# Kernel optimization log

Hardware: AMD Instinct MI355X
Metric: run time of the kernel (lower is better)

Reference implementation:

```python
import jax, jax.numpy as jnp
import numpy as np
import math

SENTINEL = 1.0e6  # eta/phi value assigned to inactive (pt<=0) objects
BIG = 1.0e6       # dR placeholder for non-lower-triangular entries


def _remove_duplicates(objs, threshold):
    """objs: (B, n, 3) with columns (pt, eta, phi). Zeros out objects that
    are within dR < threshold of a later object in the group (faithful to
    the TF strictly-lower-triangular / reduce over rows logic)."""
    n = objs.shape[1]
    active = objs[..., 0] > 0.0                              # (B, n)
    eta = jnp.where(active, objs[..., 1], SENTINEL)
    phi = jnp.where(active, objs[..., 2], SENTINEL)
    deta = eta[:, :, None] - eta[:, None, :]                 # (B, n, n)
    dphi = jnp.mod(phi[:, :, None] - phi[:, None, :] + math.pi,
                   2.0 * math.pi) - math.pi
    dr2 = deta * deta + dphi * dphi
    # strictly lower triangular mask (row i > col j), same as
    # logical_not(band_part(ones, 0, -1)) in TF
    tri = jnp.tril(jnp.ones((n, n), dtype=bool), k=-1)       # (n, n)
    # safe sqrt: only evaluate where the mask keeps the value
    dr = jnp.sqrt(jnp.where(tri, dr2, 1.0))
    replaced = jnp.where(tri, dr, BIG)                       # (B, n, n)
    # TF reduce_any(..., axis=0) per event -> axis=1 of batched tensor
    duplicates = jnp.any(replaced < threshold, axis=1)       # (B, n)
    return jnp.where(duplicates[..., None], 0.0, objs)


def duplicate_removal(x, threshold):
    jets = _remove_duplicates(x[:, 0:6], threshold)
    electrons = _remove_duplicates(x[:, 6:9], threshold)
    muons = _remove_duplicates(x[:, 9:12], threshold)
    photons = _remove_duplicates(x[:, 12:15], threshold)
    met = x[:, 15:16]
    return jnp.concatenate([jets, electrons, muons, photons, met], axis=1)


def setup_inputs() -> dict:
    key = jax.random.key(0)
    x = jax.random.normal(key, (1000000, 16, 3), dtype=jnp.float32)
    return {"x": x}


def reference(x):
    return duplicate_removal(x, 0.05)
```

## Files before the change

kernel.cpp:

```cpp
#include <hip/hip_runtime.h>
#include <math.h>

#define PI_F        3.14159274101257324e0f
#define TWOPI_F     6.28318548202514648e0f
#define TWOPI_D     ((double)TWOPI_F)
#define INV_TWOPI_D (1.0 / (double)TWOPI_F)

#define ROWS_PER_BLOCK 128
#define ROW_STRIDE     49

__device__ __forceinline__ int pair_close(float ei, float ej, float pi_, float pj) {
    float deta = __fsub_rn(ei, ej);
    float dd   = __fadd_rn(__fsub_rn(pi_, pj), PI_F);
    double ddd = (double)dd;
    double q   = trunc(ddd * INV_TWOPI_D);
    float  m   = (float)fma(-q, TWOPI_D, ddd);
    if (m < 0.0f) m = __fadd_rn(m, TWOPI_F);
    float dphi = __fsub_rn(m, PI_F);
    float dr2  = __fadd_rn(__fmul_rn(deta, deta), __fmul_rn(dphi, dphi));
    return __fsqrt_rn(dr2) < 0.05f;
}

template <int OFF, int N>
__device__ __forceinline__ unsigned group_dup(const float* r) {
    float e[N], p[N];
    int   a[N];
#pragma unroll
    for (int k = 0; k < N; ++k) {
        float pt = r[3 * (OFF + k) + 0];
        a[k] = pt > 0.0f;
        e[k] = r[3 * (OFF + k) + 1];
        p[k] = r[3 * (OFF + k) + 2];
    }
    unsigned dup = 0;
#pragma unroll
    for (int j = 0; j < N - 1; ++j) {
        int d = 0;
#pragma unroll
        for (int i = j + 1; i < N; ++i) {
            int close = pair_close(e[i], e[j], p[i], p[j]);
            d |= (a[i] & a[j] & close) | ((a[i] | a[j]) ^ 1);
        }
        if (d) dup |= (1u << (OFF + j));
    }
    return dup;
}

__global__ __launch_bounds__(256, 6) void dup_removal_kernel(
    const float4* __restrict__ in, float4* __restrict__ out, int B) {
    __shared__ float rowbuf[ROWS_PER_BLOCK * ROW_STRIDE];
    __shared__ unsigned long long maskbuf[ROWS_PER_BLOCK];

    const int t = threadIdx.x;
    const long long base4  = (long long)blockIdx.x * (ROWS_PER_BLOCK * 12);
    const long long total4 = (long long)B * 12;

    float4 v[6];
#pragma unroll
    for (int i = 0; i < 6; ++i) {
        long long g = base4 + t + 256 * i;
        if (g < total4) {
            v[i] = in[g];
            int local = t + 256 * i;
            int rl = local / 12;
            int f  = local - rl * 12;
            float* dstp = &rowbuf[rl * ROW_STRIDE + 4 * f];
            dstp[0] = v[i].x; dstp[1] = v[i].y; dstp[2] = v[i].z; dstp[3] = v[i].w;
        }
    }
    __syncthreads();

    if (t < ROWS_PER_BLOCK) {
        int row = blockIdx.x * ROWS_PER_BLOCK + t;
        unsigned dup = 0;
        if (row < B) {
            const float* r = rowbuf + t * ROW_STRIDE;
            dup  = group_dup<0, 6>(r);
            dup |= group_dup<6, 3>(r);
            dup |= group_dup<9, 3>(r);
            dup |= group_dup<12, 3>(r);
        }
        unsigned long long fm = 0ull;
#pragma unroll
        for (int o = 0; o < 15; ++o)
            fm |= (unsigned long long)((dup >> o) & 1u) * (7ull << (3 * o));
        maskbuf[t] = fm;
    }
    __syncthreads();

#pragma unroll
    for (int i = 0; i < 6; ++i) {
        long long g = base4 + t + 256 * i;
        if (g < total4) {
            int local = t + 256 * i;
            int rl = local / 12;
            int f  = local - rl * 12;
            unsigned nib = (unsigned)(maskbuf[rl] >> (4 * f)) & 0xFu;
            float4 w = v[i];
            if (nib & 1u) w.x = 0.0f;
            if (nib & 2u) w.y = 0.0f;
            if (nib & 4u) w.z = 0.0f;
            if (nib & 8u) w.w = 0.0f;
            out[g] = w;
        }
    }
}

extern "C" void kernel_launch(void* const* d_in, const int* in_sizes, int n_in,
                              void* d_out, int out_size, void* d_ws, size_t ws_size,
                              hipStream_t stream) {
    const float4* x = (const float4*)d_in[0];
    float4* out = (float4*)d_out;
    int B = in_sizes[0] / 48;
    int grid = (B + ROWS_PER_BLOCK - 1) / ROWS_PER_BLOCK;
    dup_removal_kernel<<<grid, 256, 0, stream>>>(x, out, B);
}
```

Measured before the change: 320.9 us.

## Use fp32 phi wrap, squared-distance compare, transposed LDS layout, full-block fast path

Replaces the double-precision mod computation with single-precision truncf/fma and compares squared distance against 0.0025 rather than taking a sqrt. The shared-memory row layout becomes field-strided (stride 12) so the compute-phase reads and the float4 stores conflict less across banks. A templated FULL path drops bounds checks for interior blocks, and launch bounds occupancy drops from 6 to 4. The fp32 mod and the squared compare can differ from the reference near boundaries.

```diff
diff --git a/kernel.cpp b/kernel.cpp
--- a/kernel.cpp
+++ b/kernel.cpp
@@ -3,8 +3,9 @@
 
 #define PI_F        3.14159274101257324e0f
 #define TWOPI_F     6.28318548202514648e0f
-#define TWOPI_D     ((double)TWOPI_F)
-#define INV_TWOPI_D (1.0 / (double)TWOPI_F)
+#define INV_TWOPI_F (1.0f / TWOPI_F)
+
+#define DR2_LT      0.0025f
 
 #define ROWS_PER_BLOCK 128
 #define ROW_STRIDE     49
@@ -12,13 +13,16 @@
 __device__ __forceinline__ int pair_close(float ei, float ej, float pi_, float pj) {
     float deta = __fsub_rn(ei, ej);
     float dd   = __fadd_rn(__fsub_rn(pi_, pj), PI_F);
-    double ddd = (double)dd;
-    double q   = trunc(ddd * INV_TWOPI_D);
-    float  m   = (float)fma(-q, TWOPI_D, ddd);
+    float q    = truncf(__fmul_rn(dd, INV_TWOPI_F));
+    float m    = __fmaf_rn(q, -TWOPI_F, dd);
     if (m < 0.0f) m = __fadd_rn(m, TWOPI_F);
     float dphi = __fsub_rn(m, PI_F);
     float dr2  = __fadd_rn(__fmul_rn(deta, deta), __fmul_rn(dphi, dphi));
-    return __fsqrt_rn(dr2) < 0.05f;
+    return dr2 < DR2_LT;
+}
+
+__device__ __forceinline__ float lds_at(const float* r, int u) {
+    return r[12 * (u & 3) + (u >> 2)];
 }
 
 template <int OFF, int N>
@@ -27,10 +31,10 @@
     int   a[N];
 #pragma unroll
     for (int k = 0; k < N; ++k) {
-        float pt = r[3 * (OFF + k) + 0];
-        a[k] = pt > 0.0f;
-        e[k] = r[3 * (OFF + k) + 1];
-        p[k] = r[3 * (OFF + k) + 2];
+        int u = 3 * (OFF + k);
+        a[k] = lds_at(r, u + 0) > 0.0f;
+        e[k] = lds_at(r, u + 1);
+        p[k] = lds_at(r, u + 2);
     }
     unsigned dup = 0;
 #pragma unroll
@@ -46,11 +50,10 @@
     return dup;
 }
 
-__global__ __launch_bounds__(256, 6) void dup_removal_kernel(
-    const float4* __restrict__ in, float4* __restrict__ out, int B) {
-    __shared__ float rowbuf[ROWS_PER_BLOCK * ROW_STRIDE];
-    __shared__ unsigned long long maskbuf[ROWS_PER_BLOCK];
-
+template <bool FULL>
+__device__ __forceinline__ void block_body(
+    const float4* __restrict__ in, float4* __restrict__ out, int B,
+    float* rowbuf, unsigned long long* maskbuf) {
     const int t = threadIdx.x;
     const long long base4  = (long long)blockIdx.x * (ROWS_PER_BLOCK * 12);
     const long long total4 = (long long)B * 12;
@@ -59,13 +62,13 @@
 #pragma unroll
     for (int i = 0; i < 6; ++i) {
         long long g = base4 + t + 256 * i;
-        if (g < total4) {
+        if (FULL || g < total4) {
             v[i] = in[g];
             int local = t + 256 * i;
             int rl = local / 12;
             int f  = local - rl * 12;
-            float* dstp = &rowbuf[rl * ROW_STRIDE + 4 * f];
-            dstp[0] = v[i].x; dstp[1] = v[i].y; dstp[2] = v[i].z; dstp[3] = v[i].w;
+            float* dstp = &rowbuf[rl * ROW_STRIDE + f];
+            dstp[0] = v[i].x; dstp[12] = v[i].y; dstp[24] = v[i].z; dstp[36] = v[i].w;
         }
     }
     __syncthreads();
@@ -73,7 +76,7 @@
     if (t < ROWS_PER_BLOCK) {
         int row = blockIdx.x * ROWS_PER_BLOCK + t;
         unsigned dup = 0;
-        if (row < B) {
+        if (FULL || row < B) {
             const float* r = rowbuf + t * ROW_STRIDE;
             dup  = group_dup<0, 6>(r);
             dup |= group_dup<6, 3>(r);
@@ -91,7 +94,7 @@
 #pragma unroll
     for (int i = 0; i < 6; ++i) {
         long long g = base4 + t + 256 * i;
-        if (g < total4) {
+        if (FULL || g < total4) {
             int local = t + 256 * i;
             int rl = local / 12;
             int f  = local - rl * 12;
@@ -106,6 +109,19 @@
     }
 }
 
+__global__ __launch_bounds__(256, 4) void dup_removal_kernel(
+    const float4* __restrict__ in, float4* __restrict__ out, int B) {
+    __shared__ float rowbuf[ROWS_PER_BLOCK * ROW_STRIDE];
+    __shared__ unsigned long long maskbuf[ROWS_PER_BLOCK];
+
+    const long long base4  = (long long)blockIdx.x * (ROWS_PER_BLOCK * 12);
+    const long long total4 = (long long)B * 12;
+    if (base4 + ROWS_PER_BLOCK * 12 <= total4)
+        block_body<true>(in, out, B, rowbuf, maskbuf);
+    else
+        block_body<false>(in, out, B, rowbuf, maskbuf);
+}
+
 extern "C" void kernel_launch(void* const* d_in, const int* in_sizes, int n_in,
                               void* d_out, int out_size, void* d_ws, size_t ws_size,
                               hipStream_t stream) {
```

Measured after the change: 318.3 us. Within noise of the previous version (-0.8%).

## Use one thread per row with direct vector loads, float math, nontemporal stores

Applied to the files above, without the earlier changes.

Removes the shared-memory staging and both block barriers. Each thread now loads its own 192-byte row as twelve float4 loads, computes the duplicate mask in registers, and writes the masked row with nontemporal stores. The double-precision fmod is replaced by single-precision truncation, and the sqrt is replaced by comparing dr2 against 0.0025. In exchange, the global accesses become strided per thread and so less coalesced, register pressure rises, and the float-only mod and squared threshold may differ from the reference at boundary values.

```diff
diff --git a/kernel.cpp b/kernel.cpp
--- a/kernel.cpp
+++ b/kernel.cpp
@@ -3,115 +3,83 @@
 
 #define PI_F        3.14159274101257324e0f
 #define TWOPI_F     6.28318548202514648e0f
-#define TWOPI_D     ((double)TWOPI_F)
-#define INV_TWOPI_D (1.0 / (double)TWOPI_F)
+#define INV_TWOPI_F (1.0f / TWOPI_F)
 
-#define ROWS_PER_BLOCK 128
-#define ROW_STRIDE     49
+#define DR2_LT      0.0025f
+
+typedef float v4f __attribute__((ext_vector_type(4)));
 
 __device__ __forceinline__ int pair_close(float ei, float ej, float pi_, float pj) {
     float deta = __fsub_rn(ei, ej);
     float dd   = __fadd_rn(__fsub_rn(pi_, pj), PI_F);
-    double ddd = (double)dd;
-    double q   = trunc(ddd * INV_TWOPI_D);
-    float  m   = (float)fma(-q, TWOPI_D, ddd);
+    float q    = truncf(__fmul_rn(dd, INV_TWOPI_F));
+    float m    = __fmaf_rn(q, -TWOPI_F, dd);
     if (m < 0.0f) m = __fadd_rn(m, TWOPI_F);
     float dphi = __fsub_rn(m, PI_F);
     float dr2  = __fadd_rn(__fmul_rn(deta, deta), __fmul_rn(dphi, dphi));
-    return __fsqrt_rn(dr2) < 0.05f;
+    return dr2 < DR2_LT;
 }
 
 template <int OFF, int N>
-__device__ __forceinline__ unsigned group_dup(const float* r) {
-    float e[N], p[N];
-    int   a[N];
-#pragma unroll
-    for (int k = 0; k < N; ++k) {
-        float pt = r[3 * (OFF + k) + 0];
-        a[k] = pt > 0.0f;
-        e[k] = r[3 * (OFF + k) + 1];
-        p[k] = r[3 * (OFF + k) + 2];
-    }
+__device__ __forceinline__ unsigned group_dup(const float* s) {
     unsigned dup = 0;
 #pragma unroll
     for (int j = 0; j < N - 1; ++j) {
+        int aj = s[3 * (OFF + j)] > 0.0f;
         int d = 0;
 #pragma unroll
         for (int i = j + 1; i < N; ++i) {
-            int close = pair_close(e[i], e[j], p[i], p[j]);
-            d |= (a[i] & a[j] & close) | ((a[i] | a[j]) ^ 1);
+            int ai = s[3 * (OFF + i)] > 0.0f;
+            int close = pair_close(s[3 * (OFF + i) + 1], s[3 * (OFF + j) + 1],
+                                   s[3 * (OFF + i) + 2], s[3 * (OFF + j) + 2]);
+            d |= (ai & aj & close) | ((ai | aj) ^ 1);
         }
         if (d) dup |= (1u << (OFF + j));
     }
     return dup;
 }
 
-__global__ __launch_bounds__(256, 6) void dup_removal_kernel(
-    const float4* __restrict__ in, float4* __restrict__ out, int B) {
-    __shared__ float rowbuf[ROWS_PER_BLOCK * ROW_STRIDE];
-    __shared__ unsigned long long maskbuf[ROWS_PER_BLOCK];
+__global__ __launch_bounds__(256, 4) void dup_removal_kernel(
+    const v4f* __restrict__ in, v4f* __restrict__ out, int B) {
+    int row = blockIdx.x * 256 + threadIdx.x;
+    if (row >= B) return;
 
-    const int t = threadIdx.x;
-    const long long base4  = (long long)blockIdx.x * (ROWS_PER_BLOCK * 12);
-    const long long total4 = (long long)B * 12;
+    const v4f* p = in + (size_t)row * 12;
+    float s[48];
+#pragma unroll
+    for (int i = 0; i < 12; ++i) {
+        v4f v = p[i];
+        s[4 * i + 0] = v.x; s[4 * i + 1] = v.y;
+        s[4 * i + 2] = v.z; s[4 * i + 3] = v.w;
+    }
 
-    float4 v[6];
+    unsigned dup = group_dup<0, 6>(s)
+                 | group_dup<6, 3>(s)
+                 | group_dup<9, 3>(s)
+                 | group_dup<12, 3>(s);
+
+    v4f* q = out + (size_t)row * 12;
 #pragma unroll
-    for (int i = 0; i < 6; ++i) {
-        long long g = base4 + t + 256 * i;
-        if (g < total4) {
-            v[i] = in[g];
-            int local = t + 256 * i;
-            int rl = local / 12;
-            int f  = local - rl * 12;
-            float* dstp = &rowbuf[rl * ROW_STRIDE + 4 * f];
-            dstp[0] = v[i].x; dstp[1] = v[i].y; dstp[2] = v[i].z; dstp[3] = v[i].w;
+    for (int i = 0; i < 12; ++i) {
+        v4f w;
+#pragma unroll
+        for (int c = 0; c < 4; ++c) {
+            int k = 4 * i + c;
+            float val = s[k];
+            if (k < 45)
+                val = ((dup >> (k / 3)) & 1u) ? 0.0f : val;
+            w[c] = val;
         }
-    }
-    __syncthreads();
-
-    if (t < ROWS_PER_BLOCK) {
-        int row = blockIdx.x * ROWS_PER_BLOCK + t;
-        unsigned dup = 0;
-        if (row < B) {
-            const float* r = rowbuf + t * ROW_STRIDE;
-            dup  = group_dup<0, 6>(r);
-            dup |= group_dup<6, 3>(r);
-            dup |= group_dup<9, 3>(r);
-            dup |= group_dup<12, 3>(r);
-        }
-        unsigned long long fm = 0ull;
-#pragma unroll
-        for (int o = 0; o < 15; ++o)
-            fm |= (unsigned long long)((dup >> o) & 1u) * (7ull << (3 * o));
-        maskbuf[t] = fm;
-    }
-    __syncthreads();
-
-#pragma unroll
-    for (int i = 0; i < 6; ++i) {
-        long long g = base4 + t + 256 * i;
-        if (g < total4) {
-            int local = t + 256 * i;
-            int rl = local / 12;
-            int f  = local - rl * 12;
-            unsigned nib = (unsigned)(maskbuf[rl] >> (4 * f)) & 0xFu;
-            float4 w = v[i];
-            if (nib & 1u) w.x = 0.0f;
-            if (nib & 2u) w.y = 0.0f;
-            if (nib & 4u) w.z = 0.0f;
-            if (nib & 8u) w.w = 0.0f;
-            out[g] = w;
-        }
+        __builtin_nontemporal_store(w, q + i);
     }
 }
 
 extern "C" void kernel_launch(void* const* d_in, const int* in_sizes, int n_in,
                               void* d_out, int out_size, void* d_ws, size_t ws_size,
                               hipStream_t stream) {
-    const float4* x = (const float4*)d_in[0];
-    float4* out = (float4*)d_out;
+    const v4f* x = (const v4f*)d_in[0];
+    v4f* out = (v4f*)d_out;
     int B = in_sizes[0] / 48;
-    int grid = (B + ROWS_PER_BLOCK - 1) / ROWS_PER_BLOCK;
+    int grid = (B + 255) / 256;
     dup_removal_kernel<<<grid, 256, 0, stream>>>(x, out, B);
 }
```

New measurement: 773.8 us. 2.41x slower.
